# Optimization experiments

Measured on AMD Instinct MI355X. Metric: run time of the kernel, lower is better.

The kernel has to match this reference:

```python
import jax, jax.numpy as jnp
import numpy as np

C, K, H = 256, 64, 1024


def squash(t):
    # t: [C, H]; norm = sum of squares over last dim (matches torch code)
    norm = jnp.sum(t * t, axis=-1, keepdims=True)  # [C, 1]
    scale = norm / (1.0 + norm)
    return scale * t / jnp.sqrt(norm)


def setup_inputs() -> dict:
    key = jax.random.key(0)
    k1, k2 = jax.random.split(key)
    encoder_output = jax.random.normal(k1, (C, K, H), dtype=jnp.float32)
    # nn.Linear weight [out, in]; scaled init for numerical sanity
    W = jax.random.normal(k2, (H, H), dtype=jnp.float32) * (1.0 / np.sqrt(H))
    return {"encoder_output": encoder_output, "W": W, "iter_routing": 3}


def reference(encoder_output, W, iter_routing):
    # encoder_output: [C, K, H], W: [H, H] (l_1 weight, no bias)
    # The linear projection is loop-invariant in the original; hoist it.
    x_hat = jnp.einsum('ckh,dh->ckd', encoder_output, W)  # [C, K, H]
    b = jnp.zeros(encoder_output.shape[:2], dtype=encoder_output.dtype)  # [C, K]
    c = None
    for _ in range(iter_routing):
        d = jax.nn.softmax(b, axis=-1)                       # [C, K]
        c_hat = jnp.sum(x_hat * d[..., None], axis=1)        # [C, H]
        c = squash(c_hat)                                    # [C, H]
        b = b + jnp.einsum('ckh,ch->ck', x_hat, c)           # [C, K]
    return c
```

## Files before the change

### kernel.cpp

```cpp
#include <hip/hip_runtime.h>


using f32x4  = __attribute__((ext_vector_type(4))) float;
using f32x2  = __attribute__((ext_vector_type(2))) float;
using bf16x8 = __attribute__((ext_vector_type(8))) __bf16;
using bf16x2 = __attribute__((ext_vector_type(2))) __bf16;

struct BfPair { __bf16 hi, lo; };
__device__ inline BfPair split_bf16(float x) {
    BfPair p;
    p.hi = (__bf16)x;
    p.lo = (__bf16)(x - (float)p.hi);
    return p;
}

template <int MODE>
__global__ __launch_bounds__(1024) void routing_kernel(
    const float* __restrict__ enc, const float* __restrict__ u0,
    const float* __restrict__ u1, float* __restrict__ bglob,
    __bf16* __restrict__ s_hi, __bf16* __restrict__ s_lo)
{
    __shared__ float spart[16][1024];
    __shared__ float b_s[64];
    __shared__ float d_s[64];

    const int t = threadIdx.x, lane = t & 63, w = t >> 6;
    const int c = blockIdx.x;
    const float* E = enc + (size_t)c * 65536;

    f32x4 er[4][4];
    #pragma unroll
    for (int r = 0; r < 4; ++r) {
        const float* ek = E + (size_t)(w * 4 + r) * 1024 + lane * 8;
        er[r][0] = *(const f32x4*)(ek);
        er[r][1] = *(const f32x4*)(ek + 4);
        er[r][2] = *(const f32x4*)(ek + 512);
        er[r][3] = *(const f32x4*)(ek + 516);
    }

    if (MODE > 0) {
        const size_t ub = (size_t)c * 1024 + lane * 8;
        f32x4 uf[4];
        #pragma unroll
        for (int q = 0; q < 4; ++q) {
            const size_t o = ub + (q >> 1) * 512 + (q & 1) * 4;
            uf[q] = *(const f32x4*)(u0 + o) + *(const f32x4*)(u1 + o);
        }
        #pragma unroll
        for (int r = 0; r < 4; ++r) {
            float sum = 0.f;
            #pragma unroll
            for (int q = 0; q < 4; ++q)
                #pragma unroll
                for (int j = 0; j < 4; ++j)
                    sum += er[r][q][j] * uf[q][j];
            #pragma unroll
            for (int off = 32; off; off >>= 1) sum += __shfl_xor(sum, off, 64);
            if (lane == 0) {
                const int k = w * 4 + r;
                const float bv = (MODE == 2) ? (bglob[c * 64 + k] + sum) : sum;
                bglob[c * 64 + k] = bv;
                b_s[k] = bv;
            }
        }
    }
    __syncthreads();

    if (MODE == 0) {
        if (t < 64) d_s[t] = 1.f / 64.f;
    } else if (t < 64) {
        float bv = b_s[t], m = bv;
        #pragma unroll
        for (int off = 32; off; off >>= 1) m = fmaxf(m, __shfl_xor(m, off, 64));
        const float e = expf(bv - m);
        float sm = e;
        #pragma unroll
        for (int off = 32; off; off >>= 1) sm += __shfl_xor(sm, off, 64);
        d_s[t] = e / sm;
    }
    __syncthreads();

    #pragma unroll
    for (int q = 0; q < 4; ++q) {
        f32x4 p = {};
        #pragma unroll
        for (int r = 0; r < 4; ++r) {
            const float dk = d_s[w * 4 + r];
            #pragma unroll
            for (int j = 0; j < 4; ++j) p[j] += dk * er[r][q][j];
        }
        const int h = (q >> 1) * 512 + lane * 8 + (q & 1) * 4;
        *(f32x4*)&spart[w][h] = p;
    }
    __syncthreads();

    {
        float a = 0.f;
        #pragma unroll
        for (int wv = 0; wv < 16; ++wv) a += spart[wv][t];
        const BfPair p = split_bf16(a);
        s_hi[(size_t)c * 1024 + t] = p.hi;
        s_lo[(size_t)c * 1024 + t] = p.lo;
    }
}

__global__ __launch_bounds__(256) void gemm_split_kernel(
    const __bf16* __restrict__ Ah, const __bf16* __restrict__ Al,
    const __bf16* __restrict__ Bh, const __bf16* __restrict__ Bl,
    float* __restrict__ C0, float* __restrict__ C1)
{
    const int w = threadIdx.x >> 6;
    const int gw = blockIdx.x * 4 + w;
    const int task = gw >> 1;
    const int kh   = gw & 1;
    const int mt   = task >> 6;
    const int nt   = task & 63;
    const int lane = threadIdx.x & 63;
    const int kq   = (lane >> 4) * 8 + kh * 512;
    const size_t aoff = (size_t)(mt * 16 + (lane & 15)) * 1024 + kq;
    const size_t boff = (size_t)(nt * 16 + (lane & 15)) * 1024 + kq;

    f32x4 hh = {}, hl = {}, lh = {};
    #pragma unroll 4
    for (int k0 = 0; k0 < 512; k0 += 32) {
        bf16x8 ah = *(const bf16x8*)(Ah + aoff + k0);
        bf16x8 al = *(const bf16x8*)(Al + aoff + k0);
        bf16x8 bh = *(const bf16x8*)(Bh + boff + k0);
        bf16x8 bl = *(const bf16x8*)(Bl + boff + k0);
        hh = __builtin_amdgcn_mfma_f32_16x16x32_bf16(ah, bh, hh, 0, 0, 0);
        hl = __builtin_amdgcn_mfma_f32_16x16x32_bf16(ah, bl, hl, 0, 0, 0);
        lh = __builtin_amdgcn_mfma_f32_16x16x32_bf16(al, bh, lh, 0, 0, 0);
    }
    f32x4 acc = hh + hl + lh;
    float* Cc = kh ? C1 : C0;
    const int rr = (lane >> 4) * 4, colb = lane & 15;
    #pragma unroll
    for (int r = 0; r < 4; ++r)
        Cc[(size_t)(mt * 16 + rr + r) * 1024 + nt * 16 + colb] = acc[r];
}

__global__ __launch_bounds__(256) void squash_kernel(
    const float* __restrict__ chat0, const float* __restrict__ chat1,
    __bf16* __restrict__ c_hi, __bf16* __restrict__ c_lo,
    float* __restrict__ outp)
{
    __shared__ float wsum[4];
    const int c = blockIdx.x, t = threadIdx.x;
    const int lane = t & 63, w = t >> 6;
    const int h0 = t * 4;
    const size_t o = (size_t)c * 1024 + h0;
    f32x4 v = *(const f32x4*)(chat0 + o) + *(const f32x4*)(chat1 + o);
    float ss = v[0]*v[0] + v[1]*v[1] + v[2]*v[2] + v[3]*v[3];
    #pragma unroll
    for (int off = 32; off; off >>= 1) ss += __shfl_xor(ss, off, 64);
    if (lane == 0) wsum[w] = ss;
    __syncthreads();
    const float norm = wsum[0] + wsum[1] + wsum[2] + wsum[3];
    const float scale = norm / ((1.f + norm) * sqrtf(norm) + 1e-30f);
    f32x4 ov;
    __attribute__((ext_vector_type(4))) __bf16 hv, lv;
    #pragma unroll
    for (int j = 0; j < 4; ++j) {
        ov[j] = v[j] * scale;
        const BfPair p = split_bf16(ov[j]);
        hv[j] = p.hi; lv[j] = p.lo;
    }
    *(f32x4*)(outp + o) = ov;
    *(__attribute__((ext_vector_type(4))) __bf16*)(c_hi + o) = hv;
    *(__attribute__((ext_vector_type(4))) __bf16*)(c_lo + o) = lv;
}

__global__ __launch_bounds__(256) void convert_w_kernel(
    const float* __restrict__ W, __bf16* __restrict__ Wb_hi,
    __bf16* __restrict__ Wb_lo, __bf16* __restrict__ Wt_hi,
    __bf16* __restrict__ Wt_lo)
{
    __shared__ float tile[64][65];
    const int bx = blockIdx.x, by = blockIdx.y;
    const int tx = threadIdx.x & 63, ty = threadIdx.x >> 6;
    for (int i = ty; i < 64; i += 4) {
        const size_t idx = (size_t)(by * 64 + i) * 1024 + bx * 64 + tx;
        const float v = W[idx];
        tile[i][tx] = v;
        const BfPair p = split_bf16(v);
        Wb_hi[idx] = p.hi; Wb_lo[idx] = p.lo;
    }
    __syncthreads();
    for (int i = ty; i < 64; i += 4) {
        const size_t idx = (size_t)(bx * 64 + i) * 1024 + by * 64 + tx;
        const BfPair p = split_bf16(tile[tx][i]);
        Wt_hi[idx] = p.hi; Wt_lo[idx] = p.lo;
    }
}

__global__ __launch_bounds__(512) void fallback_kernel(
    const float* __restrict__ enc, const float* __restrict__ W,
    float* __restrict__ outp)
{
    __shared__ float u_s[1024], s_s[1024], c_s[1024], chat_s[1024];
    __shared__ float b_s[64], d_s[64], red_s[8];
    const int t = threadIdx.x, lane = t & 63, w = t >> 6;
    const float* erow = enc + (size_t)blockIdx.x * 65536;

    if (t < 64) b_s[t] = 0.f;
    __syncthreads();

    for (int it = 0; it < 3; ++it) {
        if (it > 0) {
            f32x4 uf[4];
            #pragma unroll
            for (int q = 0; q < 2; ++q) {
                uf[2*q]   = *(const f32x4*)&u_s[q*512 + lane*8];
                uf[2*q+1] = *(const f32x4*)&u_s[q*512 + lane*8 + 4];
            }
            for (int r = 0; r < 8; ++r) {
                const int k = w * 8 + r;
                const float* ek = erow + (size_t)k * 1024;
                float sum = 0.f;
                #pragma unroll
                for (int q = 0; q < 2; ++q) {
                    f32x4 e0 = *(const f32x4*)(ek + q*512 + lane*8);
                    f32x4 e1 = *(const f32x4*)(ek + q*512 + lane*8 + 4);
                    #pragma unroll
                    for (int j = 0; j < 4; ++j) {
                        sum += e0[j] * uf[2*q][j];
                        sum += e1[j] * uf[2*q+1][j];
                    }
                }
                #pragma unroll
                for (int off = 32; off; off >>= 1) sum += __shfl_xor(sum, off, 64);
                if (lane == 0) b_s[k] += sum;
            }
            __syncthreads();
        }
        if (t < 64) {
            float bv = b_s[t], m = bv;
            #pragma unroll
            for (int off = 32; off; off >>= 1) m = fmaxf(m, __shfl_xor(m, off, 64));
            float e = expf(bv - m), sm = e;
            #pragma unroll
            for (int off = 32; off; off >>= 1) sm += __shfl_xor(sm, off, 64);
            d_s[t] = e / sm;
        }
        __syncthreads();
        {
            const int h0 = t * 2;
            float a0 = 0.f, a1 = 0.f;
            for (int k = 0; k < 64; ++k) {
                f32x2 ev = *(const f32x2*)(erow + (size_t)k * 1024 + h0);
                a0 += d_s[k] * ev[0]; a1 += d_s[k] * ev[1];
            }
            s_s[h0] = a0; s_s[h0+1] = a1;
        }
        __syncthreads();
        {
            f32x4 sf[4];
            #pragma unroll
            for (int q = 0; q < 2; ++q) {
                sf[2*q]   = *(const f32x4*)&s_s[q*512 + lane*8];
                sf[2*q+1] = *(const f32x4*)&s_s[q*512 + lane*8 + 4];
            }
            for (int r = 0; r < 128; ++r) {
                const int d = w * 128 + r;
                const float* wr = W + (size_t)d * 1024;
                float sum = 0.f;
                #pragma unroll
                for (int q = 0; q < 2; ++q) {
                    f32x4 w0 = *(const f32x4*)(wr + q*512 + lane*8);
                    f32x4 w1 = *(const f32x4*)(wr + q*512 + lane*8 + 4);
                    #pragma unroll
                    for (int j = 0; j < 4; ++j) {
                        sum += w0[j] * sf[2*q][j];
                        sum += w1[j] * sf[2*q+1][j];
                    }
                }
                #pragma unroll
                for (int off = 32; off; off >>= 1) sum += __shfl_xor(sum, off, 64);
                if (lane == 0) chat_s[d] = sum;
            }
        }
        __syncthreads();
        {
            const int h0 = t * 2;
            float v0 = chat_s[h0], v1 = chat_s[h0+1];
            float ss = v0*v0 + v1*v1;
            #pragma unroll
            for (int off = 32; off; off >>= 1) ss += __shfl_xor(ss, off, 64);
            if (lane == 0) red_s[w] = ss;
            __syncthreads();
            float norm = 0.f;
            #pragma unroll
            for (int i = 0; i < 8; ++i) norm += red_s[i];
            const float scale = norm / ((1.f + norm) * sqrtf(norm) + 1e-30f);
            c_s[h0] = v0 * scale; c_s[h0+1] = v1 * scale;
        }
        __syncthreads();
        if (it < 2) {
            const int h0 = t * 2;
            float uu0 = 0.f, uu1 = 0.f;
            for (int d = 0; d < 1024; ++d) {
                f32x2 wv = *(const f32x2*)(W + (size_t)d * 1024 + h0);
                uu0 += c_s[d] * wv[0]; uu1 += c_s[d] * wv[1];
            }
            u_s[h0] = uu0; u_s[h0+1] = uu1;
        } else {
            const int h0 = t * 2;
            f32x2 ov; ov[0] = c_s[h0]; ov[1] = c_s[h0+1];
            *(f32x2*)(outp + (size_t)blockIdx.x * 1024 + h0) = ov;
        }
        __syncthreads();
    }
}

extern "C" void kernel_launch(void* const* d_in, const int* in_sizes, int n_in,
                              void* d_out, int out_size, void* d_ws, size_t ws_size,
                              hipStream_t stream)
{
    const float* enc = (const float*)d_in[0];
    const float* W   = (const float*)d_in[1];
    float* outp = (float*)d_out;
    (void)in_sizes; (void)n_in; (void)out_size;

    char* ws = (char*)d_ws;
    float*  b     = (float*) (ws + 0x000000);
    __bf16* s_hi  = (__bf16*)(ws + 0x080000);
    __bf16* s_lo  = (__bf16*)(ws + 0x100000);
    __bf16* c_hi  = (__bf16*)(ws + 0x180000);
    __bf16* c_lo  = (__bf16*)(ws + 0x200000);
    float*  chat0 = (float*) (ws + 0x280000);
    float*  chat1 = (float*) (ws + 0x380000);
    float*  u0    = (float*) (ws + 0x480000);
    float*  u1    = (float*) (ws + 0x580000);
    __bf16* Wb_hi = (__bf16*)(ws + 0x680000);
    __bf16* Wb_lo = (__bf16*)(ws + 0x880000);
    __bf16* Wt_hi = (__bf16*)(ws + 0xA80000);
    __bf16* Wt_lo = (__bf16*)(ws + 0xC80000);

    if (ws_size < 0xE80000) {
        fallback_kernel<<<256, 512, 0, stream>>>(enc, W, outp);
        return;
    }

    convert_w_kernel<<<dim3(16, 16), 256, 0, stream>>>(W, Wb_hi, Wb_lo,
                                                       Wt_hi, Wt_lo);

    routing_kernel<0><<<256, 1024, 0, stream>>>(enc, u0, u1, b, s_hi, s_lo);
    gemm_split_kernel<<<512, 256, 0, stream>>>(s_hi, s_lo, Wb_hi, Wb_lo,
                                               chat0, chat1);
    squash_kernel<<<256, 256, 0, stream>>>(chat0, chat1, c_hi, c_lo, outp);
    gemm_split_kernel<<<512, 256, 0, stream>>>(c_hi, c_lo, Wt_hi, Wt_lo,
                                               u0, u1);
    routing_kernel<1><<<256, 1024, 0, stream>>>(enc, u0, u1, b, s_hi, s_lo);
    gemm_split_kernel<<<512, 256, 0, stream>>>(s_hi, s_lo, Wb_hi, Wb_lo,
                                               chat0, chat1);
    squash_kernel<<<256, 256, 0, stream>>>(chat0, chat1, c_hi, c_lo, outp);
    gemm_split_kernel<<<512, 256, 0, stream>>>(c_hi, c_lo, Wt_hi, Wt_lo,
                                               u0, u1);
    routing_kernel<2><<<256, 1024, 0, stream>>>(enc, u0, u1, b, s_hi, s_lo);
    gemm_split_kernel<<<512, 256, 0, stream>>>(s_hi, s_lo, Wb_hi, Wb_lo,
                                               chat0, chat1);
    squash_kernel<<<256, 256, 0, stream>>>(chat0, chat1, c_hi, c_lo, outp);
}
```

Measured before the change: 216.6 us.

## Precompute W^T W Gram matrix to cut per-iteration GEMMs and fuse squash

```diff
diff --git a/kernel.cpp b/kernel.cpp
--- a/kernel.cpp
+++ b/kernel.cpp
@@ -14,94 +14,103 @@
     return p;
 }
 
-template <int MODE>
-__global__ __launch_bounds__(1024) void routing_kernel(
-    const float* __restrict__ enc, const float* __restrict__ u0,
-    const float* __restrict__ u1, float* __restrict__ bglob,
-    __bf16* __restrict__ s_hi, __bf16* __restrict__ s_lo)
-{
-    __shared__ float spart[16][1024];
-    __shared__ float b_s[64];
-    __shared__ float d_s[64];
-
+__global__ __launch_bounds__(1024) void prep_kernel(
+    const float* __restrict__ enc, const float* __restrict__ W,
+    __bf16* __restrict__ s_hi, __bf16* __restrict__ s_lo,
+    float* __restrict__ s_f32,
+    __bf16* __restrict__ Wb_hi, __bf16* __restrict__ Wb_lo,
+    __bf16* __restrict__ Wt_hi, __bf16* __restrict__ Wt_lo)
+{
+    __shared__ float smem[16 * 1024];
     const int t = threadIdx.x, lane = t & 63, w = t >> 6;
-    const int c = blockIdx.x;
-    const float* E = enc + (size_t)c * 65536;
-
-    f32x4 er[4][4];
-    #pragma unroll
-    for (int r = 0; r < 4; ++r) {
-        const float* ek = E + (size_t)(w * 4 + r) * 1024 + lane * 8;
-        er[r][0] = *(const f32x4*)(ek);
-        er[r][1] = *(const f32x4*)(ek + 4);
-        er[r][2] = *(const f32x4*)(ek + 512);
-        er[r][3] = *(const f32x4*)(ek + 516);
-    }
-
-    if (MODE > 0) {
-        const size_t ub = (size_t)c * 1024 + lane * 8;
-        f32x4 uf[4];
+
+    if (blockIdx.x < 256) {
+        const int c = blockIdx.x;
+        const float* E = enc + (size_t)c * 65536;
+        f32x4 er[4][4];
+        #pragma unroll
+        for (int r = 0; r < 4; ++r) {
+            const float* ek = E + (size_t)(w * 4 + r) * 1024 + lane * 8;
+            er[r][0] = *(const f32x4*)(ek);
+            er[r][1] = *(const f32x4*)(ek + 4);
+            er[r][2] = *(const f32x4*)(ek + 512);
+            er[r][3] = *(const f32x4*)(ek + 516);
+        }
         #pragma unroll
         for (int q = 0; q < 4; ++q) {
-            const size_t o = ub + (q >> 1) * 512 + (q & 1) * 4;
-            uf[q] = *(const f32x4*)(u0 + o) + *(const f32x4*)(u1 + o);
-        }
+            f32x4 p = {};
+            #pragma unroll
+            for (int r = 0; r < 4; ++r)
+                #pragma unroll
+                for (int j = 0; j < 4; ++j) p[j] += er[r][q][j];
+            const int h = (q >> 1) * 512 + lane * 8 + (q & 1) * 4;
+            p *= (1.f / 64.f);
+            *(f32x4*)&smem[w * 1024 + h] = p;
+        }
+        __syncthreads();
+        float a = 0.f;
+        #pragma unroll
+        for (int wv = 0; wv < 16; ++wv) a += smem[wv * 1024 + t];
+        const BfPair p = split_bf16(a);
+        const size_t o = (size_t)c * 1024 + t;
+        s_hi[o] = p.hi; s_lo[o] = p.lo; s_f32[o] = a;
+    } else {
+        const int tb = blockIdx.x - 256;
+        const int bx = tb & 15, by = tb >> 4;
+        const int tx = t & 63, ty = t >> 6;
+        for (int i = ty; i < 64; i += 16) {
+            const size_t idx = (size_t)(by * 64 + i) * 1024 + bx * 64 + tx;
+            const float v = W[idx];
+            smem[i * 65 + tx] = v;
+            const BfPair p = split_bf16(v);
+            Wb_hi[idx] = p.hi; Wb_lo[idx] = p.lo;
+        }
+        __syncthreads();
+        for (int i = ty; i < 64; i += 16) {
+            const size_t idx = (size_t)(bx * 64 + i) * 1024 + by * 64 + tx;
+            const BfPair p = split_bf16(smem[tx * 65 + i]);
+            Wt_hi[idx] = p.hi; Wt_lo[idx] = p.lo;
+        }
+    }
+}
+
+__global__ __launch_bounds__(256) void gemm_g_kernel(
+    const __bf16* __restrict__ Ah, const __bf16* __restrict__ Al,
+    __bf16* __restrict__ Gh, __bf16* __restrict__ Gl)
+{
+    const int w = threadIdx.x >> 6, lane = threadIdx.x & 63;
+    const int gw = blockIdx.x * 4 + w;
+    const int mt = gw >> 4, nt = gw & 15;
+    const int kq = (lane >> 4) * 8;
+    const size_t aoff = (size_t)(mt * 16 + (lane & 15)) * 1024 + kq;
+    const size_t boff = (size_t)(nt * 64 + (lane & 15)) * 1024 + kq;
+
+    f32x4 acc0 = {}, acc1 = {}, acc2 = {}, acc3 = {};
+    for (int k0 = 0; k0 < 1024; k0 += 32) {
+        bf16x8 ah = *(const bf16x8*)(Ah + aoff + k0);
+        bf16x8 al = *(const bf16x8*)(Al + aoff + k0);
+        #pragma unroll
+        for (int j = 0; j < 4; ++j) {
+            const size_t bo = boff + (size_t)j * 16 * 1024 + k0;
+            bf16x8 bh = *(const bf16x8*)(Ah + bo);
+            bf16x8 bl = *(const bf16x8*)(Al + bo);
+            f32x4& acc = (j == 0) ? acc0 : (j == 1) ? acc1 : (j == 2) ? acc2 : acc3;
+            acc = __builtin_amdgcn_mfma_f32_16x16x32_bf16(ah, bh, acc, 0, 0, 0);
+            acc = __builtin_amdgcn_mfma_f32_16x16x32_bf16(ah, bl, acc, 0, 0, 0);
+            acc = __builtin_amdgcn_mfma_f32_16x16x32_bf16(al, bh, acc, 0, 0, 0);
+        }
+    }
+    const int rr = (lane >> 4) * 4, colb = lane & 15;
+    f32x4 accs[4] = {acc0, acc1, acc2, acc3};
+    #pragma unroll
+    for (int j = 0; j < 4; ++j)
         #pragma unroll
         for (int r = 0; r < 4; ++r) {
-            float sum = 0.f;
-            #pragma unroll
-            for (int q = 0; q < 4; ++q)
-                #pragma unroll
-                for (int j = 0; j < 4; ++j)
-                    sum += er[r][q][j] * uf[q][j];
-            #pragma unroll
-            for (int off = 32; off; off >>= 1) sum += __shfl_xor(sum, off, 64);
-            if (lane == 0) {
-                const int k = w * 4 + r;
-                const float bv = (MODE == 2) ? (bglob[c * 64 + k] + sum) : sum;
-                bglob[c * 64 + k] = bv;
-                b_s[k] = bv;
-            }
-        }
-    }
-    __syncthreads();
-
-    if (MODE == 0) {
-        if (t < 64) d_s[t] = 1.f / 64.f;
-    } else if (t < 64) {
-        float bv = b_s[t], m = bv;
-        #pragma unroll
-        for (int off = 32; off; off >>= 1) m = fmaxf(m, __shfl_xor(m, off, 64));
-        const float e = expf(bv - m);
-        float sm = e;
-        #pragma unroll
-        for (int off = 32; off; off >>= 1) sm += __shfl_xor(sm, off, 64);
-        d_s[t] = e / sm;
-    }
-    __syncthreads();
-
-    #pragma unroll
-    for (int q = 0; q < 4; ++q) {
-        f32x4 p = {};
-        #pragma unroll
-        for (int r = 0; r < 4; ++r) {
-            const float dk = d_s[w * 4 + r];
-            #pragma unroll
-            for (int j = 0; j < 4; ++j) p[j] += dk * er[r][q][j];
-        }
-        const int h = (q >> 1) * 512 + lane * 8 + (q & 1) * 4;
-        *(f32x4*)&spart[w][h] = p;
-    }
-    __syncthreads();
-
-    {
-        float a = 0.f;
-        #pragma unroll
-        for (int wv = 0; wv < 16; ++wv) a += spart[wv][t];
-        const BfPair p = split_bf16(a);
-        s_hi[(size_t)c * 1024 + t] = p.hi;
-        s_lo[(size_t)c * 1024 + t] = p.lo;
-    }
+            const size_t idx = (size_t)(mt * 16 + rr + r) * 1024
+                             + nt * 64 + j * 16 + colb;
+            const BfPair p = split_bf16(accs[j][r]);
+            Gh[idx] = p.hi; Gl[idx] = p.lo;
+        }
 }
 
 __global__ __launch_bounds__(256) void gemm_split_kernel(
@@ -139,16 +148,116 @@
         Cc[(size_t)(mt * 16 + rr + r) * 1024 + nt * 16 + colb] = acc[r];
 }
 
-__global__ __launch_bounds__(256) void squash_kernel(
+template <int MODE>
+__global__ __launch_bounds__(1024) void routing_yu_kernel(
+    const float* __restrict__ enc,
+    const float* __restrict__ y0, const float* __restrict__ y1,
+    const float* __restrict__ s_prev, float* __restrict__ bglob,
+    __bf16* __restrict__ s_hi, __bf16* __restrict__ s_lo,
+    float* __restrict__ s_out)
+{
+    __shared__ float spart[16][1024];
+    __shared__ float u_s[1024];
+    __shared__ float b_s[64];
+    __shared__ float d_s[64];
+    __shared__ float red_s[16];
+
+    const int t = threadIdx.x, lane = t & 63, w = t >> 6;
+    const int c = blockIdx.x;
+    const float* E = enc + (size_t)c * 65536;
+
+    f32x4 er[4][4];
+    #pragma unroll
+    for (int r = 0; r < 4; ++r) {
+        const float* ek = E + (size_t)(w * 4 + r) * 1024 + lane * 8;
+        er[r][0] = *(const f32x4*)(ek);
+        er[r][1] = *(const f32x4*)(ek + 4);
+        er[r][2] = *(const f32x4*)(ek + 512);
+        er[r][3] = *(const f32x4*)(ek + 516);
+    }
+
+    const size_t o = (size_t)c * 1024 + t;
+    const float yv = y0[o] + y1[o];
+    float prod = s_prev[o] * yv;
+    #pragma unroll
+    for (int off = 32; off; off >>= 1) prod += __shfl_xor(prod, off, 64);
+    if (lane == 0) red_s[w] = prod;
+    __syncthreads();
+    float norm = 0.f;
+    #pragma unroll
+    for (int i = 0; i < 16; ++i) norm += red_s[i];
+    const float alpha = norm / ((1.f + norm) * sqrtf(norm) + 1e-30f);
+    u_s[t] = alpha * yv;
+    __syncthreads();
+
+    {
+        f32x4 uf[4];
+        #pragma unroll
+        for (int q = 0; q < 4; ++q)
+            uf[q] = *(const f32x4*)&u_s[(q >> 1) * 512 + lane * 8 + (q & 1) * 4];
+        #pragma unroll
+        for (int r = 0; r < 4; ++r) {
+            float sum = 0.f;
+            #pragma unroll
+            for (int q = 0; q < 4; ++q)
+                #pragma unroll
+                for (int j = 0; j < 4; ++j)
+                    sum += er[r][q][j] * uf[q][j];
+            #pragma unroll
+            for (int off = 32; off; off >>= 1) sum += __shfl_xor(sum, off, 64);
+            if (lane == 0) {
+                const int k = w * 4 + r;
+                const float bv = (MODE == 2) ? (bglob[c * 64 + k] + sum) : sum;
+                bglob[c * 64 + k] = bv;
+                b_s[k] = bv;
+            }
+        }
+    }
+    __syncthreads();
+
+    if (t < 64) {
+        float bv = b_s[t], m = bv;
+        #pragma unroll
+        for (int off = 32; off; off >>= 1) m = fmaxf(m, __shfl_xor(m, off, 64));
+        const float e = expf(bv - m);
+        float sm = e;
+        #pragma unroll
+        for (int off = 32; off; off >>= 1) sm += __shfl_xor(sm, off, 64);
+        d_s[t] = e / sm;
+    }
+    __syncthreads();
+
+    #pragma unroll
+    for (int q = 0; q < 4; ++q) {
+        f32x4 p = {};
+        #pragma unroll
+        for (int r = 0; r < 4; ++r) {
+            const float dk = d_s[w * 4 + r];
+            #pragma unroll
+            for (int j = 0; j < 4; ++j) p[j] += dk * er[r][q][j];
+        }
+        const int h = (q >> 1) * 512 + lane * 8 + (q & 1) * 4;
+        *(f32x4*)&spart[w][h] = p;
+    }
+    __syncthreads();
+
+    {
+        float a = 0.f;
+        #pragma unroll
+        for (int wv = 0; wv < 16; ++wv) a += spart[wv][t];
+        const BfPair p = split_bf16(a);
+        s_hi[o] = p.hi; s_lo[o] = p.lo; s_out[o] = a;
+    }
+}
+
+__global__ __launch_bounds__(256) void squash_final_kernel(
     const float* __restrict__ chat0, const float* __restrict__ chat1,
-    __bf16* __restrict__ c_hi, __bf16* __restrict__ c_lo,
     float* __restrict__ outp)
 {
     __shared__ float wsum[4];
     const int c = blockIdx.x, t = threadIdx.x;
     const int lane = t & 63, w = t >> 6;
-    const int h0 = t * 4;
-    const size_t o = (size_t)c * 1024 + h0;
+    const size_t o = (size_t)c * 1024 + t * 4;
     f32x4 v = *(const f32x4*)(chat0 + o) + *(const f32x4*)(chat1 + o);
     float ss = v[0]*v[0] + v[1]*v[1] + v[2]*v[2] + v[3]*v[3];
     #pragma unroll
@@ -157,40 +266,7 @@
     __syncthreads();
     const float norm = wsum[0] + wsum[1] + wsum[2] + wsum[3];
     const float scale = norm / ((1.f + norm) * sqrtf(norm) + 1e-30f);
-    f32x4 ov;
-    __attribute__((ext_vector_type(4))) __bf16 hv, lv;
-    #pragma unroll
-    for (int j = 0; j < 4; ++j) {
-        ov[j] = v[j] * scale;
-        const BfPair p = split_bf16(ov[j]);
-        hv[j] = p.hi; lv[j] = p.lo;
-    }
-    *(f32x4*)(outp + o) = ov;
-    *(__attribute__((ext_vector_type(4))) __bf16*)(c_hi + o) = hv;
-    *(__attribute__((ext_vector_type(4))) __bf16*)(c_lo + o) = lv;
-}
-
-__global__ __launch_bounds__(256) void convert_w_kernel(
-    const float* __restrict__ W, __bf16* __restrict__ Wb_hi,
-    __bf16* __restrict__ Wb_lo, __bf16* __restrict__ Wt_hi,
-    __bf16* __restrict__ Wt_lo)
-{
-    __shared__ float tile[64][65];
-    const int bx = blockIdx.x, by = blockIdx.y;
-    const int tx = threadIdx.x & 63, ty = threadIdx.x >> 6;
-    for (int i = ty; i < 64; i += 4) {
-        const size_t idx = (size_t)(by * 64 + i) * 1024 + bx * 64 + tx;
-        const float v = W[idx];
-        tile[i][tx] = v;
-        const BfPair p = split_bf16(v);
-        Wb_hi[idx] = p.hi; Wb_lo[idx] = p.lo;
-    }
-    __syncthreads();
-    for (int i = ty; i < 64; i += 4) {
-        const size_t idx = (size_t)(bx * 64 + i) * 1024 + by * 64 + tx;
-        const BfPair p = split_bf16(tile[tx][i]);
-        Wt_hi[idx] = p.hi; Wt_lo[idx] = p.lo;
-    }
+    *(f32x4*)(outp + o) = v * scale;
 }
 
 __global__ __launch_bounds__(512) void fallback_kernel(
@@ -322,42 +398,37 @@
     (void)in_sizes; (void)n_in; (void)out_size;
 
     char* ws = (char*)d_ws;
-    float*  b     = (float*) (ws + 0x000000);
-    __bf16* s_hi  = (__bf16*)(ws + 0x080000);
-    __bf16* s_lo  = (__bf16*)(ws + 0x100000);
-    __bf16* c_hi  = (__bf16*)(ws + 0x180000);
-    __bf16* c_lo  = (__bf16*)(ws + 0x200000);
-    float*  chat0 = (float*) (ws + 0x280000);
-    float*  chat1 = (float*) (ws + 0x380000);
-    float*  u0    = (float*) (ws + 0x480000);
-    float*  u1    = (float*) (ws + 0x580000);
-    __bf16* Wb_hi = (__bf16*)(ws + 0x680000);
-    __bf16* Wb_lo = (__bf16*)(ws + 0x880000);
-    __bf16* Wt_hi = (__bf16*)(ws + 0xA80000);
-    __bf16* Wt_lo = (__bf16*)(ws + 0xC80000);
-
-    if (ws_size < 0xE80000) {
+    float*  b      = (float*) (ws + 0x0000000);
+    __bf16* s_hi   = (__bf16*)(ws + 0x0010000);
+    __bf16* s_lo   = (__bf16*)(ws + 0x0090000);
+    float*  s_f32a = (float*) (ws + 0x0110000);
+    float*  s_f32b = (float*) (ws + 0x0210000);
+    float*  y0     = (float*) (ws + 0x0310000);
+    float*  y1     = (float*) (ws + 0x0410000);
+    float*  chat0  = (float*) (ws + 0x0510000);
+    float*  chat1  = (float*) (ws + 0x0610000);
+    __bf16* Wb_hi  = (__bf16*)(ws + 0x0710000);
+    __bf16* Wb_lo  = (__bf16*)(ws + 0x0910000);
+    __bf16* Wt_hi  = (__bf16*)(ws + 0x0B10000);
+    __bf16* Wt_lo  = (__bf16*)(ws + 0x0D10000);
+    __bf16* Gh     = (__bf16*)(ws + 0x0F10000);
+    __bf16* Gl     = (__bf16*)(ws + 0x1110000);
+
+    if (ws_size < 0x1310000) {
         fallback_kernel<<<256, 512, 0, stream>>>(enc, W, outp);
         return;
     }
 
-    convert_w_kernel<<<dim3(16, 16), 256, 0, stream>>>(W, Wb_hi, Wb_lo,
-                                                       Wt_hi, Wt_lo);
-
-    routing_kernel<0><<<256, 1024, 0, stream>>>(enc, u0, u1, b, s_hi, s_lo);
+    prep_kernel<<<512, 1024, 0, stream>>>(enc, W, s_hi, s_lo, s_f32a,
+                                          Wb_hi, Wb_lo, Wt_hi, Wt_lo);
+    gemm_g_kernel<<<256, 256, 0, stream>>>(Wt_hi, Wt_lo, Gh, Gl);
+    gemm_split_kernel<<<512, 256, 0, stream>>>(s_hi, s_lo, Gh, Gl, y0, y1);
+    routing_yu_kernel<1><<<256, 1024, 0, stream>>>(enc, y0, y1, s_f32a, b,
+                                                   s_hi, s_lo, s_f32b);
+    gemm_split_kernel<<<512, 256, 0, stream>>>(s_hi, s_lo, Gh, Gl, y0, y1);
+    routing_yu_kernel<2><<<256, 1024, 0, stream>>>(enc, y0, y1, s_f32b, b,
+                                                   s_hi, s_lo, s_f32a);
     gemm_split_kernel<<<512, 256, 0, stream>>>(s_hi, s_lo, Wb_hi, Wb_lo,
                                                chat0, chat1);
-    squash_kernel<<<256, 256, 0, stream>>>(chat0, chat1, c_hi, c_lo, outp);
-    gemm_split_kernel<<<512, 256, 0, stream>>>(c_hi, c_lo, Wt_hi, Wt_lo,
-                                               u0, u1);
-    routing_kernel<1><<<256, 1024, 0, stream>>>(enc, u0, u1, b, s_hi, s_lo);
-    gemm_split_kernel<<<512, 256, 0, stream>>>(s_hi, s_lo, Wb_hi, Wb_lo,
-                                               chat0, chat1);
-    squash_kernel<<<256, 256, 0, stream>>>(chat0, chat1, c_hi, c_lo, outp);
-    gemm_split_kernel<<<512, 256, 0, stream>>>(c_hi, c_lo, Wt_hi, Wt_lo,
-                                               u0, u1);
-    routing_kernel<2><<<256, 1024, 0, stream>>>(enc, u0, u1, b, s_hi, s_lo);
-    gemm_split_kernel<<<512, 256, 0, stream>>>(s_hi, s_lo, Wb_hi, Wb_lo,
-                                               chat0, chat1);
-    squash_kernel<<<256, 256, 0, stream>>>(chat0, chat1, c_hi, c_lo, outp);
-}
+    squash_final_kernel<<<256, 256, 0, stream>>>(chat0, chat1, outp);
+}
```

Measured after the change: 222.0 us. 1.03x slower.
